# Kernel tuning notes

Hardware: AMD Instinct MI355X
Metric: run time of the kernel (lower is better)

## Reference

```python
import jax, jax.numpy as jnp
import numpy as np

EPS = 1e-5  # torch InstanceNorm2d default eps


def setup_inputs() -> dict:
    key = jax.random.key(0)
    ks = jax.random.split(key, 5)
    B, C, H, W = 4, 64, 64, 64
    x = jax.random.normal(ks[0], (B, C, H, W), dtype=jnp.float32)
    # Conv2d 1x1 weights as [out_c, in_c] matrices (kernel dims squeezed)
    w_qkv = jax.random.normal(ks[1], (3 * C, C), dtype=jnp.float32) * (C ** -0.5)
    b_qkv = jax.random.normal(ks[2], (3 * C,), dtype=jnp.float32) * 0.02
    w_proj = jax.random.normal(ks[3], (C, C), dtype=jnp.float32) * (C ** -0.5)
    b_proj = jax.random.normal(ks[4], (C,), dtype=jnp.float32) * 0.02
    return {"x": x, "w_qkv": w_qkv, "b_qkv": b_qkv, "w_proj": w_proj, "b_proj": b_proj}


def reference(x, w_qkv, b_qkv, w_proj, b_proj):
    B, C, H, W = x.shape
    scale = C ** -0.5
    # InstanceNorm2d(affine=False): per-(B,C) stats over spatial dims, biased var
    mean = jnp.mean(x, axis=(2, 3), keepdims=True)
    var = jnp.var(x, axis=(2, 3), keepdims=True)
    h = (x - mean) * jax.lax.rsqrt(var + EPS)
    # 1x1 conv qkv projection: [B,3C,H,W]
    qkv = jnp.einsum('bchw,oc->bohw', h, w_qkv) + b_qkv[None, :, None, None]
    q, k, v = jnp.split(qkv, 3, axis=1)
    HW = H * W
    q = q.reshape(B, C, HW).transpose(0, 2, 1)  # [B, HW, C]
    k = k.reshape(B, C, HW)                      # [B, C, HW]
    v = v.reshape(B, C, HW).transpose(0, 2, 1)  # [B, HW, C]
    attn = jnp.einsum('bnc,bcm->bnm', q, k) * scale  # [B, HW, HW]
    attn = jax.nn.softmax(attn, axis=-1)
    # dropout p=0.0 -> identity
    h = jnp.einsum('bnm,bmc->bnc', attn, v)          # [B, HW, C]
    h = h.transpose(0, 2, 1).reshape(B, C, H, W)
    h = jnp.einsum('bchw,oc->bohw', h, w_proj) + b_proj[None, :, None, None]
    return x + h
```

## Files before the change

kernel.cpp:

```cpp
#include <hip/hip_runtime.h>
#include <hip/hip_bf16.h>

#define B_ 4
#define C_ 64
#define N_ 4096
#define EPS_ 1e-5f
#define C2_ 0.18033688011112042f

typedef __hip_bfloat16 bf16;
typedef __attribute__((ext_vector_type(8))) short short8;
typedef __attribute__((ext_vector_type(4))) short short4v;
typedef __attribute__((ext_vector_type(4))) float f32x4;

__device__ __forceinline__ float b2f(bf16 v) { return __bfloat162float(v); }

__device__ __forceinline__ short f2bs(float f) {
  union { bf16 h; short s; } u;
  u.h = __float2bfloat16(f);
  return u.s;
}

__device__ __forceinline__ short8 pk8(const float* f) {
  union { short8 v; short s[8]; } u;
#pragma unroll
  for (int i = 0; i < 8; ++i) u.s[i] = f2bs(f[i]);
  return u.v;
}

__device__ __forceinline__ void up8(short8 v, float* d) {
  union { short8 v; unsigned u[4]; } x;
  x.v = v;
  d[0] = __uint_as_float(x.u[0] << 16);
  d[1] = __uint_as_float(x.u[0] & 0xffff0000u);
  d[2] = __uint_as_float(x.u[1] << 16);
  d[3] = __uint_as_float(x.u[1] & 0xffff0000u);
  d[4] = __uint_as_float(x.u[2] << 16);
  d[5] = __uint_as_float(x.u[2] & 0xffff0000u);
  d[6] = __uint_as_float(x.u[3] << 16);
  d[7] = __uint_as_float(x.u[3] & 0xffff0000u);
}

__device__ __forceinline__ void up4(ushort4 u, float* d) {
  d[0] = __uint_as_float(((unsigned)u.x) << 16);
  d[1] = __uint_as_float(((unsigned)u.y) << 16);
  d[2] = __uint_as_float(((unsigned)u.z) << 16);
  d[3] = __uint_as_float(((unsigned)u.w) << 16);
}

template <bool F32>
__device__ __forceinline__ float ldx(const void* p, size_t idx) {
  if (F32) return ((const float*)p)[idx];
  return b2f(((const bf16*)p)[idx]);
}

template <bool F32>
__device__ __forceinline__ short8 ld8(const void* p, int idx) {
  if (F32) {
    const float* fp = (const float*)p + idx;
    float tmp[8];
    *(float4*)&tmp[0] = *(const float4*)fp;
    *(float4*)&tmp[4] = *(const float4*)(fp + 4);
    return pk8(tmp);
  }
  return *(const short8*)((const bf16*)p + idx);
}

__device__ __forceinline__ f32x4 mfma32(short8 a, short8 b, f32x4 c) {
  return __builtin_amdgcn_mfma_f32_16x16x32_bf16(a, b, c, 0, 0, 0);
}
__device__ __forceinline__ f32x4 mfma16(short4v a, short4v b, f32x4 c) {
  return __builtin_amdgcn_mfma_f32_16x16x16bf16_1k(a, b, c, 0, 0, 0);
}


template <bool F32>
__device__ __forceinline__ void stats_sum(const void* x, int bc, int t,
                                          float& s, float& s2) {
  if (F32) {
    const float4* xp = (const float4*)((const float*)x + (size_t)bc * N_);
#pragma unroll
    for (int r = 0; r < 4; ++r) {
      const float4 v = xp[r * 256 + t];
      s += (v.x + v.y) + (v.z + v.w);
      s2 += (v.x * v.x + v.y * v.y) + (v.z * v.z + v.w * v.w);
    }
  } else {
    const bf16* xp = (const bf16*)x + (size_t)bc * N_;
#pragma unroll
    for (int r = 0; r < 2; ++r) {
      float f[8];
      up8(*(const short8*)(xp + (r * 256 + t) * 8), f);
#pragma unroll
      for (int i = 0; i < 8; ++i) { s += f[i]; s2 += f[i] * f[i]; }
    }
  }
}

__global__ __launch_bounds__(256) void k_stats(const void* __restrict__ x,
                                               float* __restrict__ meanArr,
                                               float* __restrict__ rstdArr,
                                               int* __restrict__ flag) {
  const int bc = blockIdx.x, t = threadIdx.x;
  __shared__ float ps[4], ps2[4];
  __shared__ int pflag;
  {
    const ushort* xw = (const ushort*)x + (size_t)bc * 4096;
    int cnt = 0;
#pragma unroll
    for (int j = 0; j < 4; ++j) {
      const ushort4 u = *(const ushort4*)(xw + t * 16 + j * 4);
      cnt += ((u.x >> 7) & 0xFF) >= 143;
      cnt += ((u.y >> 7) & 0xFF) >= 143;
      cnt += ((u.z >> 7) & 0xFF) >= 143;
      cnt += ((u.w >> 7) & 0xFF) >= 143;
    }
#pragma unroll
    for (int off = 32; off > 0; off >>= 1) cnt += __shfl_down(cnt, off, 64);
    if (t == 0) pflag = 0;
    __syncthreads();
    if ((t & 63) == 0 && cnt > 16) atomicAdd(&pflag, cnt);
    __syncthreads();
  }
  const bool f32 = pflag > 64;
  float s = 0.f, s2 = 0.f;
  if (f32) stats_sum<true>(x, bc, t, s, s2);
  else stats_sum<false>(x, bc, t, s, s2);
#pragma unroll
  for (int off = 32; off > 0; off >>= 1) {
    s += __shfl_down(s, off, 64);
    s2 += __shfl_down(s2, off, 64);
  }
  if ((t & 63) == 0) { ps[t >> 6] = s; ps2[t >> 6] = s2; }
  __syncthreads();
  if (t == 0) {
    const float S = (ps[0] + ps[1]) + (ps[2] + ps[3]);
    const float S2 = (ps2[0] + ps2[1]) + (ps2[2] + ps2[3]);
    const float mean = S * (1.0f / N_);
    const float var = S2 * (1.0f / N_) - mean * mean;
    meanArr[bc] = mean;
    rstdArr[bc] = rsqrtf(var + EPS_);
    flag[0] = f32 ? 1 : 0;
  }
}

template <bool F32>
__device__ __forceinline__ void qkv_body(const void* x, const void* wqkv,
                                         const void* bqkv, const float* meanArr,
                                         const float* rstdArr, bf16* q, bf16* k,
                                         bf16* v, short* HB) {
  const int t = threadIdx.x, tj16 = blockIdx.x, b = blockIdx.y;
  const int n0 = tj16 * 16;
  {
    const int li = t & 15, cg = t >> 4;
#pragma unroll
    for (int i = 0; i < 4; ++i) {
      const int c = cg * 4 + i;
      const float xv = ldx<F32>(x, ((size_t)(b * 64 + c)) * N_ + n0 + li);
      const float hv = (xv - meanArr[b * 64 + c]) * rstdArr[b * 64 + c];
      HB[((c >> 5) * 64 + ((c >> 3) & 3) * 16 + li) * 8 + (c & 7)] = f2bs(hv);
    }
  }
  __syncthreads();
  const int l = t & 63, w = t >> 6, li = l & 15, quad = l >> 4;
  short8 Wf[3][2];
#pragma unroll
  for (int sec = 0; sec < 3; ++sec)
#pragma unroll
    for (int ks = 0; ks < 2; ++ks)
      Wf[sec][ks] =
          ld8<F32>(wqkv, (sec * 64 + w * 16 + li) * 64 + ks * 32 + quad * 8);
  short8 Hf[2];
#pragma unroll
  for (int ks = 0; ks < 2; ++ks)
    Hf[ks] = *(const short8*)&HB[(ks * 64 + l) * 8];
  float bq[4], bk[4];
#pragma unroll
  for (int r = 0; r < 4; ++r) {
    bq[r] = ldx<F32>(bqkv, w * 16 + quad * 4 + r);
    bk[r] = ldx<F32>(bqkv, 64 + w * 16 + quad * 4 + r);
  }
  const float bv = ldx<F32>(bqkv, 128 + w * 16 + li);
  f32x4 dq = {0.f, 0.f, 0.f, 0.f}, dk = dq, dv = dq;
  dq = mfma32(Wf[0][0], Hf[0], dq);
  dq = mfma32(Wf[0][1], Hf[1], dq);
  dk = mfma32(Wf[1][0], Hf[0], dk);
  dk = mfma32(Wf[1][1], Hf[1], dk);
  dv = mfma32(Hf[0], Wf[2][0], dv);
  dv = mfma32(Hf[1], Wf[2][1], dv);
  union { ushort4 u; short s[4]; } pq, pk_, pv;
#pragma unroll
  for (int r = 0; r < 4; ++r) {
    pq.s[r] = f2bs((dq[r] + bq[r]) * C2_);
    pk_.s[r] = f2bs(dk[r] + bk[r]);
    pv.s[r] = f2bs(dv[r] + bv);
  }
  const int lhi = ((w & 1) * 2 + (quad >> 1)) * 16 + li;
  const int jj0 = (quad & 1) * 4;
  *(ushort4*)&q[(((size_t)(b * 256 + tj16)) * 2 + (w >> 1)) * 512 + lhi * 8 + jj0] = pq.u;
  *(ushort4*)&k[(((size_t)(b * 64 + (tj16 >> 2))) * 8 + (tj16 & 3) * 2 + (w >> 1)) * 512 + lhi * 8 + jj0] = pk_.u;
  *(ushort4*)&v[(((size_t)(b * 64 + (tj16 >> 2))) * 8 + w * 2 + ((tj16 >> 1) & 1)) * 512 + l * 8 + (tj16 & 1) * 4] = pv.u;
}
__global__ __launch_bounds__(256, 4) void k_qkv(
    const void* __restrict__ x, const void* __restrict__ wqkv,
    const void* __restrict__ bqkv, const float* __restrict__ meanArr,
    const float* __restrict__ rstdArr, bf16* __restrict__ q,
    bf16* __restrict__ k, bf16* __restrict__ v, const int* __restrict__ flag) {
  __shared__ short HB[1024];
  if (*flag) qkv_body<true>(x, wqkv, bqkv, meanArr, rstdArr, q, k, v, HB);
  else qkv_body<false>(x, wqkv, bqkv, meanArr, rstdArr, q, k, v, HB);
}

__device__ __forceinline__ void stage(short* dst, const bf16* ks_,
                                      const bf16* vs_, int w, int ln) {
#pragma unroll
  for (int i = 0; i < 2; ++i) {
    const int off = w * 1024 + i * 512;
    __builtin_amdgcn_global_load_lds(
        (const __attribute__((address_space(1))) unsigned int*)(ks_ + off + ln * 8),
        (__attribute__((address_space(3))) unsigned int*)(dst + off), 16, 0, 0);
    __builtin_amdgcn_global_load_lds(
        (const __attribute__((address_space(1))) unsigned int*)(vs_ + off + ln * 8),
        (__attribute__((address_space(3))) unsigned int*)(dst + 4096 + off), 16, 0, 0);
  }
}

__global__ __launch_bounds__(256, 4) void k_attn(
    const bf16* __restrict__ qg, const bf16* __restrict__ kg,
    const bf16* __restrict__ vg, bf16* __restrict__ opart,
    float* __restrict__ lpart) {
  __shared__ __align__(16) short KV[2][8192];
  const int bid = blockIdx.x;
  const int kh = bid & 7, b = (bid >> 3) & 3, qt = bid >> 5;
  const int t = threadIdx.x, l = t & 63, w = t >> 6, li = l & 15;

  short8 Qf[2][2];
#pragma unroll
  for (int q = 0; q < 2; ++q)
#pragma unroll
    for (int ks = 0; ks < 2; ++ks)
      Qf[q][ks] = *(const short8*)(qg +
          (((size_t)(b * 256 + qt * 8 + w * 2 + q)) * 2 + ks) * 512 + l * 8);

  f32x4 O[4][2];
#pragma unroll
  for (int cb = 0; cb < 4; ++cb)
#pragma unroll
    for (int q = 0; q < 2; ++q) O[cb][q] = {0.f, 0.f, 0.f, 0.f};
  float ls[2] = {0.f, 0.f};

  const bf16* kbase = kg + ((size_t)(b * 64 + kh * 8)) * 4096;
  const bf16* vbase = vg + ((size_t)(b * 64 + kh * 8)) * 4096;

  stage(&KV[0][0], kbase, vbase, w, l);
  __syncthreads();
  for (int it = 0; it < 8; ++it) {
    const short* buf = &KV[it & 1][0];
    if (it + 1 < 8)
      stage(&KV[(it + 1) & 1][0], kbase + (size_t)(it + 1) * 4096,
            vbase + (size_t)(it + 1) * 4096, w, l);
#pragma unroll
    for (int jp = 0; jp < 2; ++jp) {
      short8 Vp[4];
#pragma unroll
      for (int cb = 0; cb < 4; ++cb)
        Vp[cb] = *(const short8*)&buf[4096 + (cb * 2 + jp) * 512 + l * 8];
#pragma unroll
      for (int jh = 0; jh < 2; ++jh) {
        const int jb = jp * 2 + jh;
        const short8 Kf0 = *(const short8*)&buf[(jb * 2 + 0) * 512 + l * 8];
        const short8 Kf1 = *(const short8*)&buf[(jb * 2 + 1) * 512 + l * 8];
        short4v Pf[2];
#pragma unroll
        for (int q = 0; q < 2; ++q) {
          f32x4 sv = {0.f, 0.f, 0.f, 0.f};
          sv = mfma32(Kf0, Qf[q][0], sv);
          sv = mfma32(Kf1, Qf[q][1], sv);
          const float p0 = exp2f(sv[0]), p1 = exp2f(sv[1]);
          const float p2 = exp2f(sv[2]), p3 = exp2f(sv[3]);
          ls[q] += (p0 + p1) + (p2 + p3);
          union { short4v v; __hip_bfloat162 h[2]; } pu;
          pu.h[0] = __float22bfloat162_rn(make_float2(p0, p1));
          pu.h[1] = __float22bfloat162_rn(make_float2(p2, p3));
          Pf[q] = pu.v;
        }
#pragma unroll
        for (int cb = 0; cb < 4; ++cb) {
          const short4v vh = jh
              ? __builtin_shufflevector(Vp[cb], Vp[cb], 4, 5, 6, 7)
              : __builtin_shufflevector(Vp[cb], Vp[cb], 0, 1, 2, 3);
          O[cb][0] = mfma16(vh, Pf[0], O[cb][0]);
          O[cb][1] = mfma16(vh, Pf[1], O[cb][1]);
        }
      }
    }
    __syncthreads();
  }
#pragma unroll
  for (int q = 0; q < 2; ++q) {
    ls[q] += __shfl_xor(ls[q], 16, 64);
    ls[q] += __shfl_xor(ls[q], 32, 64);
  }
  const size_t pb = ((size_t)(kh * 4 + b)) * 32 + qt;
  if (l < 16) {
#pragma unroll
    for (int q = 0; q < 2; ++q)
      lpart[(pb * 8 + w * 2 + q) * 16 + l] = ls[q];
  }
#pragma unroll
  for (int q = 0; q < 2; ++q)
#pragma unroll
    for (int cb = 0; cb < 4; ++cb) {
      union { ushort4 u; short s[4]; } pk_;
#pragma unroll
      for (int r = 0; r < 4; ++r) pk_.s[r] = f2bs(O[cb][q][r]);
      *(ushort4*)&opart[((pb * 8 + w * 2 + q) * 4 + cb) * 256 + l * 4] = pk_.u;
    }
}

template <bool F32>
__device__ __forceinline__ void proj_body(const bf16* opart, const float* lpart,
                                          const void* xg, const void* wp,
                                          const void* bp, void* outv) {
  const int bx = blockIdx.x, bb = blockIdx.y;
  const int sub = bx & 3, qt64 = bx >> 2;
  const int qt = qt64 >> 1;
  const int t = threadIdx.x, l = t & 63, w = t >> 6, li = l & 15, quad = l >> 4;
  short8 Wa[2];
#pragma unroll
  for (int ks = 0; ks < 2; ++ks)
    Wa[ks] = ld8<F32>(wp, (w * 16 + li) * 64 + ks * 32 + quad * 8);
  float bpv[4];
#pragma unroll
  for (int r = 0; r < 4; ++r) bpv[r] = ldx<F32>(bp, w * 16 + quad * 4 + r);
  const int mbg = (qt64 & 1) * 4 + sub;
  float lv = 0.f;
#pragma unroll
  for (int p = 0; p < 8; ++p)
    lv += lpart[((((size_t)(p * 4 + bb)) * 32 + qt) * 8 + mbg) * 16 + li];
  lv = 1.0f / lv;
  f32x4 acc = {0.f, 0.f, 0.f, 0.f};
#pragma unroll
  for (int ks = 0; ks < 2; ++ks) {
    const int cb = ks * 2 + (quad >> 1);
    const int qs0 = (quad & 1) * 2;
    float s8[8] = {};
#pragma unroll
    for (int p = 0; p < 8; ++p) {
      const size_t base =
          (((((size_t)(p * 4 + bb)) * 32 + qt) * 8 + mbg) * 4 + cb) * 256;
      float f0[4], f1[4];
      up4(*(const ushort4*)&opart[base + (qs0 * 16 + li) * 4], f0);
      up4(*(const ushort4*)&opart[base + ((qs0 + 1) * 16 + li) * 4], f1);
#pragma unroll
      for (int i = 0; i < 4; ++i) { s8[i] += f0[i]; s8[4 + i] += f1[i]; }
    }
#pragma unroll
    for (int i = 0; i < 8; ++i) s8[i] *= lv;
    acc = mfma32(Wa[ks], pk8(s8), acc);
  }
#pragma unroll
  for (int r = 0; r < 4; ++r) {
    const int o = w * 16 + quad * 4 + r;
    const int n = qt64 * 64 + sub * 16 + li;
    const size_t idx = ((size_t)(bb * 64 + o)) * N_ + n;
    const float res = ldx<F32>(xg, idx) + acc[r] + bpv[r];
    if (F32) ((float*)outv)[idx] = res;
    else ((bf16*)outv)[idx] = __float2bfloat16(res);
  }
}
__global__ __launch_bounds__(256, 4) void k_proj(
    const bf16* __restrict__ opart, const float* __restrict__ lpart,
    const void* __restrict__ xg, const void* __restrict__ wp,
    const void* __restrict__ bp, void* __restrict__ outv,
    const int* __restrict__ flag) {
  if (*flag) proj_body<true>(opart, lpart, xg, wp, bp, outv);
  else proj_body<false>(opart, lpart, xg, wp, bp, outv);
}

extern "C" void kernel_launch(void* const* d_in, const int* in_sizes, int n_in,
                              void* d_out, int out_size, void* d_ws,
                              size_t ws_size, hipStream_t stream) {
  const void* x = d_in[0];
  const void* wqkv = d_in[1];
  const void* bqkv = d_in[2];
  const void* wproj = d_in[3];
  const void* bproj = d_in[4];

  char* ws = (char*)d_ws;
  float* meanArr = (float*)ws;
  float* rstdArr = (float*)(ws + 1024);
  int* flag = (int*)(ws + 2048);
  bf16* q = (bf16*)(ws + 4096);
  bf16* k = (bf16*)(ws + 4096 + (2u << 20));
  bf16* v = (bf16*)(ws + 4096 + (4u << 20));
  bf16* opart = (bf16*)(ws + 4096 + (6u << 20));
  float* lpart = (float*)(ws + 4096 + (22u << 20));

  k_stats<<<256, 256, 0, stream>>>(x, meanArr, rstdArr, flag);
  k_qkv<<<dim3(256, 4), 256, 0, stream>>>(x, wqkv, bqkv, meanArr, rstdArr, q,
                                          k, v, flag);
  k_attn<<<1024, 256, 0, stream>>>(q, k, v, opart, lpart);
  k_proj<<<dim3(256, 4), 256, 0, stream>>>(opart, lpart, x, wproj, bproj,
                                           d_out, flag);
}
```

Baseline: 116.1 us.

## Fuse four kernels into one persistent kernel with grid-wide atomic barriers

Replaces the stats, qkv, attention and projection launches with a single 512-block kernel whose phases are separated by atomic-counter grid barriers. Each block runs two qkv and two proj jobs, and the attention split-K factor drops from 8 to 4 key chunks, with each block looping over 16 tiles instead of 8. This removes three launch gaps and halves the partial-output traffic reduced in proj. In exchange it relies on all 512 blocks being co-resident, since the barriers would deadlock otherwise. It also gives attention fewer, longer blocks and adds a memset launch to reset the counters.

```diff
diff --git a/kernel.cpp b/kernel.cpp
--- a/kernel.cpp
+++ b/kernel.cpp
@@ -72,12 +72,28 @@
   return __builtin_amdgcn_mfma_f32_16x16x16bf16_1k(a, b, c, 0, 0, 0);
 }
 
+__device__ __forceinline__ void gbar(unsigned* cnt, int idx, unsigned tgt) {
+  __syncthreads();
+  if (threadIdx.x == 0) {
+    __threadfence();
+    atomicAdd(&cnt[idx], 1u);
+    while (__hip_atomic_load(&cnt[idx], __ATOMIC_RELAXED,
+                             __HIP_MEMORY_SCOPE_AGENT) < tgt) {
+      __builtin_amdgcn_s_sleep(2);
+    }
+    __threadfence();
+  }
+  __syncthreads();
+}
 
 template <bool F32>
-__device__ __forceinline__ void stats_sum(const void* x, int bc, int t,
-                                          float& s, float& s2) {
+__device__ __forceinline__ void stats_phase(const void* x, float* meanArr,
+                                            float* rstdArr, int g, int t,
+                                            float* lds) {
+  if (g >= 256) return;
+  float s = 0.f, s2 = 0.f;
   if (F32) {
-    const float4* xp = (const float4*)((const float*)x + (size_t)bc * N_);
+    const float4* xp = (const float4*)((const float*)x + (size_t)g * N_);
 #pragma unroll
     for (int r = 0; r < 4; ++r) {
       const float4 v = xp[r * 256 + t];
@@ -85,7 +101,7 @@
       s2 += (v.x * v.x + v.y * v.y) + (v.z * v.z + v.w * v.w);
     }
   } else {
-    const bf16* xp = (const bf16*)x + (size_t)bc * N_;
+    const bf16* xp = (const bf16*)x + (size_t)g * N_;
 #pragma unroll
     for (int r = 0; r < 2; ++r) {
       float f[8];
@@ -94,42 +110,13 @@
       for (int i = 0; i < 8; ++i) { s += f[i]; s2 += f[i] * f[i]; }
     }
   }
-}
-
-__global__ __launch_bounds__(256) void k_stats(const void* __restrict__ x,
-                                               float* __restrict__ meanArr,
-                                               float* __restrict__ rstdArr,
-                                               int* __restrict__ flag) {
-  const int bc = blockIdx.x, t = threadIdx.x;
-  __shared__ float ps[4], ps2[4];
-  __shared__ int pflag;
-  {
-    const ushort* xw = (const ushort*)x + (size_t)bc * 4096;
-    int cnt = 0;
-#pragma unroll
-    for (int j = 0; j < 4; ++j) {
-      const ushort4 u = *(const ushort4*)(xw + t * 16 + j * 4);
-      cnt += ((u.x >> 7) & 0xFF) >= 143;
-      cnt += ((u.y >> 7) & 0xFF) >= 143;
-      cnt += ((u.z >> 7) & 0xFF) >= 143;
-      cnt += ((u.w >> 7) & 0xFF) >= 143;
-    }
-#pragma unroll
-    for (int off = 32; off > 0; off >>= 1) cnt += __shfl_down(cnt, off, 64);
-    if (t == 0) pflag = 0;
-    __syncthreads();
-    if ((t & 63) == 0 && cnt > 16) atomicAdd(&pflag, cnt);
-    __syncthreads();
-  }
-  const bool f32 = pflag > 64;
-  float s = 0.f, s2 = 0.f;
-  if (f32) stats_sum<true>(x, bc, t, s, s2);
-  else stats_sum<false>(x, bc, t, s, s2);
 #pragma unroll
   for (int off = 32; off > 0; off >>= 1) {
     s += __shfl_down(s, off, 64);
     s2 += __shfl_down(s2, off, 64);
   }
+  float* ps = lds;
+  float* ps2 = lds + 4;
   if ((t & 63) == 0) { ps[t >> 6] = s; ps2[t >> 6] = s2; }
   __syncthreads();
   if (t == 0) {
@@ -137,19 +124,19 @@
     const float S2 = (ps2[0] + ps2[1]) + (ps2[2] + ps2[3]);
     const float mean = S * (1.0f / N_);
     const float var = S2 * (1.0f / N_) - mean * mean;
-    meanArr[bc] = mean;
-    rstdArr[bc] = rsqrtf(var + EPS_);
-    flag[0] = f32 ? 1 : 0;
+    meanArr[g] = mean;
+    rstdArr[g] = rsqrtf(var + EPS_);
   }
 }
 
 template <bool F32>
-__device__ __forceinline__ void qkv_body(const void* x, const void* wqkv,
-                                         const void* bqkv, const float* meanArr,
-                                         const float* rstdArr, bf16* q, bf16* k,
-                                         bf16* v, short* HB) {
-  const int t = threadIdx.x, tj16 = blockIdx.x, b = blockIdx.y;
+__device__ __forceinline__ void qkv_job(const void* x, const void* wqkv,
+                                        const void* bqkv, const float* meanArr,
+                                        const float* rstdArr, bf16* q, bf16* k,
+                                        bf16* v, int job, int t, short* HB) {
+  const int b = job & 3, tj16 = job >> 2;
   const int n0 = tj16 * 16;
+  __syncthreads();
   {
     const int li = t & 15, cg = t >> 4;
 #pragma unroll
@@ -200,15 +187,6 @@
   *(ushort4*)&k[(((size_t)(b * 64 + (tj16 >> 2))) * 8 + (tj16 & 3) * 2 + (w >> 1)) * 512 + lhi * 8 + jj0] = pk_.u;
   *(ushort4*)&v[(((size_t)(b * 64 + (tj16 >> 2))) * 8 + w * 2 + ((tj16 >> 1) & 1)) * 512 + l * 8 + (tj16 & 1) * 4] = pv.u;
 }
-__global__ __launch_bounds__(256, 4) void k_qkv(
-    const void* __restrict__ x, const void* __restrict__ wqkv,
-    const void* __restrict__ bqkv, const float* __restrict__ meanArr,
-    const float* __restrict__ rstdArr, bf16* __restrict__ q,
-    bf16* __restrict__ k, bf16* __restrict__ v, const int* __restrict__ flag) {
-  __shared__ short HB[1024];
-  if (*flag) qkv_body<true>(x, wqkv, bqkv, meanArr, rstdArr, q, k, v, HB);
-  else qkv_body<false>(x, wqkv, bqkv, meanArr, rstdArr, q, k, v, HB);
-}
 
 __device__ __forceinline__ void stage(short* dst, const bf16* ks_,
                                       const bf16* vs_, int w, int ln) {
@@ -224,14 +202,12 @@
   }
 }
 
-__global__ __launch_bounds__(256, 4) void k_attn(
-    const bf16* __restrict__ qg, const bf16* __restrict__ kg,
-    const bf16* __restrict__ vg, bf16* __restrict__ opart,
-    float* __restrict__ lpart) {
-  __shared__ __align__(16) short KV[2][8192];
-  const int bid = blockIdx.x;
-  const int kh = bid & 7, b = (bid >> 3) & 3, qt = bid >> 5;
-  const int t = threadIdx.x, l = t & 63, w = t >> 6, li = l & 15;
+__device__ __forceinline__ void attn_phase(const bf16* qg, const bf16* kg,
+                                           const bf16* vg, bf16* opart,
+                                           float* lpart, int g, int t,
+                                           short* KVp) {
+  const int kh = g & 3, b = (g >> 2) & 3, qt = g >> 4;
+  const int l = t & 63, w = t >> 6, li = l & 15;
 
   short8 Qf[2][2];
 #pragma unroll
@@ -248,15 +224,15 @@
     for (int q = 0; q < 2; ++q) O[cb][q] = {0.f, 0.f, 0.f, 0.f};
   float ls[2] = {0.f, 0.f};
 
-  const bf16* kbase = kg + ((size_t)(b * 64 + kh * 8)) * 4096;
-  const bf16* vbase = vg + ((size_t)(b * 64 + kh * 8)) * 4096;
-
-  stage(&KV[0][0], kbase, vbase, w, l);
-  __syncthreads();
-  for (int it = 0; it < 8; ++it) {
-    const short* buf = &KV[it & 1][0];
-    if (it + 1 < 8)
-      stage(&KV[(it + 1) & 1][0], kbase + (size_t)(it + 1) * 4096,
+  const bf16* kbase = kg + ((size_t)(b * 64 + kh * 16)) * 4096;
+  const bf16* vbase = vg + ((size_t)(b * 64 + kh * 16)) * 4096;
+
+  stage(KVp, kbase, vbase, w, l);
+  __syncthreads();
+  for (int it = 0; it < 16; ++it) {
+    const short* buf = KVp + (it & 1) * 8192;
+    if (it + 1 < 16)
+      stage(KVp + ((it + 1) & 1) * 8192, kbase + (size_t)(it + 1) * 4096,
             vbase + (size_t)(it + 1) * 4096, w, l);
 #pragma unroll
     for (int jp = 0; jp < 2; ++jp) {
@@ -318,13 +294,14 @@
 }
 
 template <bool F32>
-__device__ __forceinline__ void proj_body(const bf16* opart, const float* lpart,
-                                          const void* xg, const void* wp,
-                                          const void* bp, void* outv) {
-  const int bx = blockIdx.x, bb = blockIdx.y;
+__device__ __forceinline__ void proj_job(const bf16* opart, const float* lpart,
+                                         const void* xg, const void* wp,
+                                         const void* bp, void* outv, int job,
+                                         int t) {
+  const int bb = job & 3, bx = job >> 2;
   const int sub = bx & 3, qt64 = bx >> 2;
   const int qt = qt64 >> 1;
-  const int t = threadIdx.x, l = t & 63, w = t >> 6, li = l & 15, quad = l >> 4;
+  const int l = t & 63, w = t >> 6, li = l & 15, quad = l >> 4;
   short8 Wa[2];
 #pragma unroll
   for (int ks = 0; ks < 2; ++ks)
@@ -335,7 +312,7 @@
   const int mbg = (qt64 & 1) * 4 + sub;
   float lv = 0.f;
 #pragma unroll
-  for (int p = 0; p < 8; ++p)
+  for (int p = 0; p < 4; ++p)
     lv += lpart[((((size_t)(p * 4 + bb)) * 32 + qt) * 8 + mbg) * 16 + li];
   lv = 1.0f / lv;
   f32x4 acc = {0.f, 0.f, 0.f, 0.f};
@@ -345,7 +322,7 @@
     const int qs0 = (quad & 1) * 2;
     float s8[8] = {};
 #pragma unroll
-    for (int p = 0; p < 8; ++p) {
+    for (int p = 0; p < 4; ++p) {
       const size_t base =
           (((((size_t)(p * 4 + bb)) * 32 + qt) * 8 + mbg) * 4 + cb) * 256;
       float f0[4], f1[4];
@@ -368,13 +345,56 @@
     else ((bf16*)outv)[idx] = __float2bfloat16(res);
   }
 }
-__global__ __launch_bounds__(256, 4) void k_proj(
-    const bf16* __restrict__ opart, const float* __restrict__ lpart,
-    const void* __restrict__ xg, const void* __restrict__ wp,
-    const void* __restrict__ bp, void* __restrict__ outv,
-    const int* __restrict__ flag) {
-  if (*flag) proj_body<true>(opart, lpart, xg, wp, bp, outv);
-  else proj_body<false>(opart, lpart, xg, wp, bp, outv);
+
+__global__ __launch_bounds__(256, 2) void k_mega(
+    const void* __restrict__ x, const void* __restrict__ wqkv,
+    const void* __restrict__ bqkv, const void* __restrict__ wproj,
+    const void* __restrict__ bproj, void* __restrict__ outv,
+    float* __restrict__ meanArr, float* __restrict__ rstdArr,
+    bf16* __restrict__ q, bf16* __restrict__ k, bf16* __restrict__ v,
+    bf16* __restrict__ opart, float* __restrict__ lpart,
+    unsigned* __restrict__ cnt) {
+  __shared__ __align__(16) short KV[2][8192];
+  const int g = blockIdx.x, t = threadIdx.x;
+
+  bool f32;
+  {
+    const ushort* xw = (const ushort*)x;
+    const ushort4 u = *(const ushort4*)(xw + (size_t)g * 1024 + t * 4);
+    int c = (((u.x >> 7) & 0xFF) >= 143) + (((u.y >> 7) & 0xFF) >= 143) +
+            (((u.z >> 7) & 0xFF) >= 143) + (((u.w >> 7) & 0xFF) >= 143);
+#pragma unroll
+    for (int off = 32; off > 0; off >>= 1) c += __shfl_down(c, off, 64);
+    int* pc = (int*)&KV[0][0];
+    if ((t & 63) == 0) pc[t >> 6] = c;
+    __syncthreads();
+    f32 = (pc[0] + pc[1] + pc[2] + pc[3]) > 64;
+    __syncthreads();
+  }
+
+  if (f32) stats_phase<true>(x, meanArr, rstdArr, g, t, (float*)&KV[0][0]);
+  else stats_phase<false>(x, meanArr, rstdArr, g, t, (float*)&KV[0][0]);
+  gbar(cnt, 0, 512);
+
+  if (f32) {
+    qkv_job<true>(x, wqkv, bqkv, meanArr, rstdArr, q, k, v, 2 * g, t, &KV[0][0]);
+    qkv_job<true>(x, wqkv, bqkv, meanArr, rstdArr, q, k, v, 2 * g + 1, t, &KV[0][0]);
+  } else {
+    qkv_job<false>(x, wqkv, bqkv, meanArr, rstdArr, q, k, v, 2 * g, t, &KV[0][0]);
+    qkv_job<false>(x, wqkv, bqkv, meanArr, rstdArr, q, k, v, 2 * g + 1, t, &KV[0][0]);
+  }
+  gbar(cnt, 1, 512);
+
+  attn_phase(q, k, v, opart, lpart, g, t, &KV[0][0]);
+  gbar(cnt, 2, 512);
+
+  if (f32) {
+    proj_job<true>(opart, lpart, x, wproj, bproj, outv, 2 * g, t);
+    proj_job<true>(opart, lpart, x, wproj, bproj, outv, 2 * g + 1, t);
+  } else {
+    proj_job<false>(opart, lpart, x, wproj, bproj, outv, 2 * g, t);
+    proj_job<false>(opart, lpart, x, wproj, bproj, outv, 2 * g + 1, t);
+  }
 }
 
 extern "C" void kernel_launch(void* const* d_in, const int* in_sizes, int n_in,
@@ -385,21 +405,20 @@
   const void* bqkv = d_in[2];
   const void* wproj = d_in[3];
   const void* bproj = d_in[4];
+  void* outp = d_out;
 
   char* ws = (char*)d_ws;
   float* meanArr = (float*)ws;
   float* rstdArr = (float*)(ws + 1024);
-  int* flag = (int*)(ws + 2048);
-  bf16* q = (bf16*)(ws + 4096);
-  bf16* k = (bf16*)(ws + 4096 + (2u << 20));
-  bf16* v = (bf16*)(ws + 4096 + (4u << 20));
+  unsigned* cnt = (unsigned*)(ws + 2048);
+  bf16* qb = (bf16*)(ws + 4096);
+  bf16* kb = (bf16*)(ws + 4096 + (2u << 20));
+  bf16* vb = (bf16*)(ws + 4096 + (4u << 20));
   bf16* opart = (bf16*)(ws + 4096 + (6u << 20));
-  float* lpart = (float*)(ws + 4096 + (22u << 20));
-
-  k_stats<<<256, 256, 0, stream>>>(x, meanArr, rstdArr, flag);
-  k_qkv<<<dim3(256, 4), 256, 0, stream>>>(x, wqkv, bqkv, meanArr, rstdArr, q,
-                                          k, v, flag);
-  k_attn<<<1024, 256, 0, stream>>>(q, k, v, opart, lpart);
-  k_proj<<<dim3(256, 4), 256, 0, stream>>>(opart, lpart, x, wproj, bproj,
-                                           d_out, flag);
-}
+  float* lpart = (float*)(ws + 4096 + (14u << 20));
+
+  hipMemsetAsync(cnt, 0, 64, stream);
+  k_mega<<<512, 256, 0, stream>>>(x, wqkv, bqkv, wproj, bproj, outp, meanArr,
+                                  rstdArr, qb, kb, vb, opart, lpart,
+                                  (unsigned*)cnt);
+}
```

Result: slower. 251.9 us (+117.0%).
